# Optimization experiments

Hardware: AMD Instinct MI355X
Metric: run time of the kernel (lower is better)

## Reference

```python
import jax, jax.numpy as jnp
import numpy as np


def setup_inputs() -> dict:
    key = jax.random.key(0)
    k1, k2 = jax.random.split(key)
    B, D, H, W = 64, 64, 32, 32
    K = 1024
    z_e = jax.random.normal(k1, (B, D, H, W), dtype=jnp.float32)
    embedding = jax.random.normal(k2, (K, D), dtype=jnp.float32)
    return {"z_e": z_e, "embedding": embedding}


def reference(z_e, embedding):
    # Eval-mode forward of VectorQuantizer (EMA buffer updates are training-only state).
    B, D, H, W = z_e.shape
    K = embedding.shape[0]
    # (N, D) flattened encoder outputs, N = B*H*W
    flat = jnp.transpose(z_e, (0, 2, 3, 1)).reshape(-1, D)
    dist = (jnp.sum(flat * flat, axis=1, keepdims=True)
            + jnp.sum(embedding * embedding, axis=1)
            - 2.0 * flat @ embedding.T)  # (N, K)
    indices = jnp.argmin(dist, axis=1)  # (N,)
    z_q_flat = embedding[indices]  # (N, D) gather
    z_q = jnp.transpose(z_q_flat.reshape(B, H, W, D), (0, 3, 1, 2))
    # commitment loss: mse(z_e, sg(z_q))
    commitment_loss = jnp.mean((z_e - jax.lax.stop_gradient(z_q)) ** 2)
    # straight-through estimator
    z_q = z_e + jax.lax.stop_gradient(z_q - z_e)
    indices_bhw = indices.reshape(B, H, W)
    # fraction of codebook entries used this batch (jit-friendly unique count)
    used = jnp.zeros((K,), dtype=jnp.float32).at[indices].set(1.0)
    codebook_usage = jnp.sum(used) / K
    return z_q, commitment_loss, indices_bhw, codebook_usage
```

## Files before the change

### kernel.cpp

```cpp
#include <hip/hip_runtime.h>


#define DIMS 64
#define K_CODES 1024
#define N_QUERIES 65536
#define HW 1024
#define TOTAL_ELEMS 4194304
#define PLANE 4096

typedef __attribute__((ext_vector_type(8))) short v8s;
typedef __attribute__((ext_vector_type(4))) float f32x4;

__device__ inline unsigned short f2bf(float x) {
    union { float f; unsigned u; } v; v.f = x;
    unsigned r = v.u + 0x7fff + ((v.u >> 16) & 1);
    return (unsigned short)(r >> 16);
}
__device__ inline float bf2f(unsigned short h) {
    union { unsigned u; float f; } v; v.u = ((unsigned)h) << 16; return v.f;
}

__global__ void vq_prep(const float* __restrict__ emb, float* __restrict__ ws_norm,
                        int* __restrict__ ws_flags, float* __restrict__ ws_loss) {
    int k = blockIdx.x * 256 + threadIdx.x;
    const float4* row = (const float4*)(emb + k * DIMS);
    float s = 0.f;
#pragma unroll
    for (int i = 0; i < 16; ++i) {
        float4 v = row[i];
        s += v.x * v.x + v.y * v.y + v.z * v.z + v.w * v.w;
    }
    ws_norm[k] = s;
    ws_flags[k] = 0;
    if (k == 0) *ws_loss = 0.f;
}

#define MFMA16(A_, B_, C_) __builtin_amdgcn_mfma_f32_16x16x32_bf16(A_, B_, C_, 0, 0, 0)

__global__ __launch_bounds__(256, 2)
void vq_main(const float* __restrict__ z_e, const float* __restrict__ emb,
             const float* __restrict__ ws_norm, int* __restrict__ ws_flags,
             float* __restrict__ ws_loss, float* __restrict__ out) {
    __shared__ unsigned short ldsB[2][3 * PLANE];
    __shared__ int   fIdx[128];
    __shared__ float wsum[4];

    const int tid  = threadIdx.x;
    const int lane = tid & 63;
    const int wid  = tid >> 6;
    const int qbase = blockIdx.x * 128;
    const int b    = qbase >> 10;
    const int hwb  = qbase & (HW - 1);

    const int col  = lane & 15;
    const int qd   = lane >> 4;

    v8s afr[2][2][3];
    {
        const float* zb = z_e + b * (DIMS * HW);
#pragma unroll
        for (int rt = 0; rt < 2; ++rt) {
            int hwq = hwb + wid * 32 + rt * 16 + col;
#pragma unroll
            for (int kc = 0; kc < 2; ++kc) {
                int dbase = kc * 32 + qd * 8;
#pragma unroll
                for (int j = 0; j < 8; ++j) {
                    float x = zb[(dbase + j) * HW + hwq];
                    unsigned short h = f2bf(x);  float r1 = x - bf2f(h);
                    unsigned short m = f2bf(r1); float r2 = r1 - bf2f(m);
                    afr[rt][kc][0][j] = (short)h;
                    afr[rt][kc][1][j] = (short)m;
                    afr[rt][kc][2][j] = (short)f2bf(r2);
                }
            }
        }
    }

    float bestv[2][4];
    int   besti[2][4];
#pragma unroll
    for (int rt = 0; rt < 2; ++rt)
#pragma unroll
        for (int r = 0; r < 4; ++r) { bestv[rt][r] = 3.4e38f; besti[rt][r] = 0; }

    float4 regs[4];

    auto stage_loads = [&](int t) {
        const float4* src = (const float4*)(emb + t * 64 * DIMS);
#pragma unroll
        for (int i = 0; i < 4; ++i) regs[i] = src[tid + 256 * i];
    };
    auto stage_write = [&](int bb) {
        unsigned short* dst = &ldsB[bb][0];
#pragma unroll
        for (int i = 0; i < 4; ++i) {
            int e    = (tid + 256 * i) * 4;
            int code = e >> 6;
            int d    = e & 63;
            int o    = d >> 3;
            int sub  = d & 7;
            float xs[4] = {regs[i].x, regs[i].y, regs[i].z, regs[i].w};
            unsigned short h[4], mm_[4], l[4];
#pragma unroll
            for (int q = 0; q < 4; ++q) {
                float x = xs[q];
                unsigned short hh = f2bf(x);  float r1 = x - bf2f(hh);
                unsigned short mh = f2bf(r1); float r2 = r1 - bf2f(mh);
                h[q] = hh; mm_[q] = mh; l[q] = f2bf(r2);
            }
            int base = (o * 64 + code) * 8 + sub;
            uint2 uh, um, ul;
            uh.x = (unsigned)h[0]   | ((unsigned)h[1] << 16);
            uh.y = (unsigned)h[2]   | ((unsigned)h[3] << 16);
            um.x = (unsigned)mm_[0] | ((unsigned)mm_[1] << 16);
            um.y = (unsigned)mm_[2] | ((unsigned)mm_[3] << 16);
            ul.x = (unsigned)l[0]   | ((unsigned)l[1] << 16);
            ul.y = (unsigned)l[2]   | ((unsigned)l[3] << 16);
            *(uint2*)(dst + base)             = uh;
            *(uint2*)(dst + PLANE + base)     = um;
            *(uint2*)(dst + 2 * PLANE + base) = ul;
        }
    };

    stage_loads(0);
    stage_write(0);
    __syncthreads();

    for (int t = 0; t < 16; ++t) {
        const int cur = t & 1;
        if (t < 15) stage_loads(t + 1);
        const unsigned short* bufc = &ldsB[cur][0];
#pragma unroll
        for (int cs = 0; cs < 4; ++cs) {
            float nrm = ws_norm[t * 64 + cs * 16 + col];
            v8s bfr[2][3];
#pragma unroll
            for (int kc = 0; kc < 2; ++kc)
#pragma unroll
                for (int p = 0; p < 3; ++p)
                    bfr[kc][p] = *(const v8s*)(bufc + p * PLANE +
                                 (((kc * 4 + qd) * 64) + cs * 16 + col) * 8);
            f32x4 acc0 = {0.f, 0.f, 0.f, 0.f};
            f32x4 acc1 = {0.f, 0.f, 0.f, 0.f};
#pragma unroll
            for (int kc = 0; kc < 2; ++kc) {
                acc0 = MFMA16(afr[0][kc][0], bfr[kc][0], acc0);
                acc1 = MFMA16(afr[1][kc][0], bfr[kc][0], acc1);
                acc0 = MFMA16(afr[0][kc][0], bfr[kc][1], acc0);
                acc1 = MFMA16(afr[1][kc][0], bfr[kc][1], acc1);
                acc0 = MFMA16(afr[0][kc][1], bfr[kc][0], acc0);
                acc1 = MFMA16(afr[1][kc][1], bfr[kc][0], acc1);
                acc0 = MFMA16(afr[0][kc][1], bfr[kc][1], acc0);
                acc1 = MFMA16(afr[1][kc][1], bfr[kc][1], acc1);
                acc0 = MFMA16(afr[0][kc][0], bfr[kc][2], acc0);
                acc1 = MFMA16(afr[1][kc][0], bfr[kc][2], acc1);
                acc0 = MFMA16(afr[0][kc][2], bfr[kc][0], acc0);
                acc1 = MFMA16(afr[1][kc][2], bfr[kc][0], acc1);
            }
            int cbase = t * 64 + cs * 16 + col;
#pragma unroll
            for (int r = 0; r < 4; ++r) {
                float d0 = fmaf(-2.f, acc0[r], nrm);
                if (d0 < bestv[0][r]) { bestv[0][r] = d0; besti[0][r] = cbase; }
                float d1 = fmaf(-2.f, acc1[r], nrm);
                if (d1 < bestv[1][r]) { bestv[1][r] = d1; besti[1][r] = cbase; }
            }
        }
        if (t < 15) stage_write(1 - cur);
        __syncthreads();
    }

#pragma unroll
    for (int rt = 0; rt < 2; ++rt)
#pragma unroll
    for (int r = 0; r < 4; ++r) {
        float v = bestv[rt][r];
        int   idx = besti[rt][r];
#pragma unroll
        for (int m = 8; m >= 1; m >>= 1) {
            float ov = __shfl_xor(v, m, 64);
            int   oi = __shfl_xor(idx, m, 64);
            if (ov < v || (ov == v && oi < idx)) { v = ov; idx = oi; }
        }
        if (col == 0) {
            int q = wid * 32 + rt * 16 + qd * 4 + r;
            fIdx[q] = idx;
            out[TOTAL_ELEMS + 1 + qbase + q] = (float)idx;
            ws_flags[idx] = 1;
        }
    }
    __syncthreads();

    const int q  = tid & 127;
    const int dh = tid >> 7;
    const int n  = qbase + q;
    const int bb = n >> 10;
    const int hw = n & (HW - 1);
    const int myIdx = fIdx[q];
    const float* erow = emb + myIdx * DIMS;
    float lsum = 0.f;
#pragma unroll
    for (int it = 0; it < 32; ++it) {
        int d = it * 2 + dh;
        float v = erow[d];
        int   o = bb * (DIMS * HW) + d * HW + hw;
        float ze = z_e[o];
        out[o] = v;
        float df = ze - v;
        lsum = fmaf(df, df, lsum);
    }
#pragma unroll
    for (int off = 32; off > 0; off >>= 1) lsum += __shfl_down(lsum, off, 64);
    if (lane == 0) wsum[wid] = lsum;
    __syncthreads();
    if (tid == 0) atomicAdd(ws_loss, wsum[0] + wsum[1] + wsum[2] + wsum[3]);
}

__global__ void vq_final(const int* __restrict__ flags, const float* __restrict__ loss,
                         float* __restrict__ out) {
    __shared__ int cnt[256];
    int tid = threadIdx.x;
    int c = flags[tid] + flags[tid + 256] + flags[tid + 512] + flags[tid + 768];
    cnt[tid] = c;
    __syncthreads();
    for (int s = 128; s > 0; s >>= 1) {
        if (tid < s) cnt[tid] += cnt[tid + s];
        __syncthreads();
    }
    if (tid == 0) {
        out[TOTAL_ELEMS] = *loss / (float)TOTAL_ELEMS;
        out[TOTAL_ELEMS + 1 + N_QUERIES] = (float)cnt[0] / (float)K_CODES;
    }
}

extern "C" void kernel_launch(void* const* d_in, const int* in_sizes, int n_in,
                              void* d_out, int out_size, void* d_ws, size_t ws_size,
                              hipStream_t stream) {
    const float* z_e = (const float*)d_in[0];
    const float* emb = (const float*)d_in[1];
    float* out = (float*)d_out;
    float* ws_norm  = (float*)d_ws;
    int*   ws_flags = (int*)((char*)d_ws + 4096);
    float* ws_loss  = (float*)((char*)d_ws + 8192);

    vq_prep<<<4, 256, 0, stream>>>(emb, ws_norm, ws_flags, ws_loss);
    vq_main<<<512, 256, 0, stream>>>(z_e, emb, ws_norm, ws_flags, ws_loss, out);
    vq_final<<<1, 256, 0, stream>>>(ws_flags, ws_loss, out);
}
```

Baseline: 135.4 us.

## Fuse final reduction into main kernel, double block size, swizzle LDS codebook layout

Each block now has 512 threads and handles 256 queries, so a block stages each codebook tile once for twice as many queries. The B-operand LDS layout gets an XOR swizzle to reduce bank conflicts. The LDS write for the next tile is moved into the middle of the compute loop to overlap with MFMA work. Codebook usage becomes a per-block shared bitmask merged with atomicOr. A last-block-done counter computes the final loss and usage inside the main kernel, which removes the separate final launch. The cost is half as many blocks (256), which lowers parallelism across CUs, plus a thread fence and atomic counter per block.

```diff
diff --git a/kernel.cpp b/kernel.cpp
--- a/kernel.cpp
+++ b/kernel.cpp
@@ -7,6 +7,8 @@
 #define HW 1024
 #define TOTAL_ELEMS 4194304
 #define PLANE 4096
+#define NBLK 256
+#define QPB 256
 
 typedef __attribute__((ext_vector_type(8))) short v8s;
 typedef __attribute__((ext_vector_type(4))) float f32x4;
@@ -21,7 +23,8 @@
 }
 
 __global__ void vq_prep(const float* __restrict__ emb, float* __restrict__ ws_norm,
-                        int* __restrict__ ws_flags, float* __restrict__ ws_loss) {
+                        unsigned* __restrict__ ws_flags, float* __restrict__ ws_loss,
+                        int* __restrict__ ws_cnt) {
     int k = blockIdx.x * 256 + threadIdx.x;
     const float4* row = (const float4*)(emb + k * DIMS);
     float s = 0.f;
@@ -31,29 +34,34 @@
         s += v.x * v.x + v.y * v.y + v.z * v.z + v.w * v.w;
     }
     ws_norm[k] = s;
-    ws_flags[k] = 0;
-    if (k == 0) *ws_loss = 0.f;
+    if (k < 32) ws_flags[k] = 0u;
+    if (k == 0) { *ws_loss = 0.f; *ws_cnt = 0; }
 }
 
 #define MFMA16(A_, B_, C_) __builtin_amdgcn_mfma_f32_16x16x32_bf16(A_, B_, C_, 0, 0, 0)
 
-__global__ __launch_bounds__(256, 2)
+__global__ __launch_bounds__(512, 2)
 void vq_main(const float* __restrict__ z_e, const float* __restrict__ emb,
-             const float* __restrict__ ws_norm, int* __restrict__ ws_flags,
-             float* __restrict__ ws_loss, float* __restrict__ out) {
+             const float* __restrict__ ws_norm, unsigned* __restrict__ ws_flags,
+             float* __restrict__ ws_loss, int* __restrict__ ws_cnt,
+             float* __restrict__ out) {
     __shared__ unsigned short ldsB[2][3 * PLANE];
-    __shared__ int   fIdx[128];
-    __shared__ float wsum[4];
+    __shared__ int      fIdx[QPB];
+    __shared__ float    wsum[8];
+    __shared__ unsigned umask[32];
+    __shared__ int      lastBlk;
 
     const int tid  = threadIdx.x;
     const int lane = tid & 63;
     const int wid  = tid >> 6;
-    const int qbase = blockIdx.x * 128;
+    const int qbase = blockIdx.x * QPB;
     const int b    = qbase >> 10;
     const int hwb  = qbase & (HW - 1);
 
     const int col  = lane & 15;
     const int qd   = lane >> 4;
+
+    if (tid < 32) umask[tid] = 0u;
 
     v8s afr[2][2][3];
     {
@@ -84,18 +92,17 @@
 #pragma unroll
         for (int r = 0; r < 4; ++r) { bestv[rt][r] = 3.4e38f; besti[rt][r] = 0; }
 
-    float4 regs[4];
-
+    float4 regs[2];
     auto stage_loads = [&](int t) {
         const float4* src = (const float4*)(emb + t * 64 * DIMS);
 #pragma unroll
-        for (int i = 0; i < 4; ++i) regs[i] = src[tid + 256 * i];
+        for (int i = 0; i < 2; ++i) regs[i] = src[tid + 512 * i];
     };
-    auto stage_write = [&](int bb) {
-        unsigned short* dst = &ldsB[bb][0];
-#pragma unroll
-        for (int i = 0; i < 4; ++i) {
-            int e    = (tid + 256 * i) * 4;
+    auto stage_write = [&](int bb2) {
+        unsigned short* dst = &ldsB[bb2][0];
+#pragma unroll
+        for (int i = 0; i < 2; ++i) {
+            int e    = (tid + 512 * i) * 4;
             int code = e >> 6;
             int d    = e & 63;
             int o    = d >> 3;
@@ -109,7 +116,7 @@
                 unsigned short mh = f2bf(r1); float r2 = r1 - bf2f(mh);
                 h[q] = hh; mm_[q] = mh; l[q] = f2bf(r2);
             }
-            int base = (o * 64 + code) * 8 + sub;
+            int base = (o * 64 + (code ^ (o << 1))) * 8 + sub;
             uint2 uh, um, ul;
             uh.x = (unsigned)h[0]   | ((unsigned)h[1] << 16);
             uh.y = (unsigned)h[2]   | ((unsigned)h[3] << 16);
@@ -131,16 +138,18 @@
         const int cur = t & 1;
         if (t < 15) stage_loads(t + 1);
         const unsigned short* bufc = &ldsB[cur][0];
-#pragma unroll
-        for (int cs = 0; cs < 4; ++cs) {
+
+        auto csbody = [&](int cs) {
             float nrm = ws_norm[t * 64 + cs * 16 + col];
             v8s bfr[2][3];
 #pragma unroll
-            for (int kc = 0; kc < 2; ++kc)
+            for (int kc = 0; kc < 2; ++kc) {
+                int oct = kc * 4 + qd;
+                int slot = (cs * 16 + col) ^ (oct << 1);
 #pragma unroll
                 for (int p = 0; p < 3; ++p)
-                    bfr[kc][p] = *(const v8s*)(bufc + p * PLANE +
-                                 (((kc * 4 + qd) * 64) + cs * 16 + col) * 8);
+                    bfr[kc][p] = *(const v8s*)(bufc + p * PLANE + (oct * 64 + slot) * 8);
+            }
             f32x4 acc0 = {0.f, 0.f, 0.f, 0.f};
             f32x4 acc1 = {0.f, 0.f, 0.f, 0.f};
 #pragma unroll
@@ -166,8 +175,13 @@
                 float d1 = fmaf(-2.f, acc1[r], nrm);
                 if (d1 < bestv[1][r]) { bestv[1][r] = d1; besti[1][r] = cbase; }
             }
-        }
+        };
+
+        csbody(0);
+        csbody(1);
         if (t < 15) stage_write(1 - cur);
+        csbody(2);
+        csbody(3);
         __syncthreads();
     }
 
@@ -187,13 +201,13 @@
             int q = wid * 32 + rt * 16 + qd * 4 + r;
             fIdx[q] = idx;
             out[TOTAL_ELEMS + 1 + qbase + q] = (float)idx;
-            ws_flags[idx] = 1;
-        }
-    }
-    __syncthreads();
-
-    const int q  = tid & 127;
-    const int dh = tid >> 7;
+            atomicOr(&umask[idx >> 5], 1u << (idx & 31));
+        }
+    }
+    __syncthreads();
+
+    const int q  = tid & (QPB - 1);
+    const int dh = tid >> 8;
     const int n  = qbase + q;
     const int bb = n >> 10;
     const int hw = n & (HW - 1);
@@ -214,23 +228,29 @@
     for (int off = 32; off > 0; off >>= 1) lsum += __shfl_down(lsum, off, 64);
     if (lane == 0) wsum[wid] = lsum;
     __syncthreads();
-    if (tid == 0) atomicAdd(ws_loss, wsum[0] + wsum[1] + wsum[2] + wsum[3]);
-}
-
-__global__ void vq_final(const int* __restrict__ flags, const float* __restrict__ loss,
-                         float* __restrict__ out) {
-    __shared__ int cnt[256];
-    int tid = threadIdx.x;
-    int c = flags[tid] + flags[tid + 256] + flags[tid + 512] + flags[tid + 768];
-    cnt[tid] = c;
-    __syncthreads();
-    for (int s = 128; s > 0; s >>= 1) {
-        if (tid < s) cnt[tid] += cnt[tid + s];
-        __syncthreads();
-    }
+
+    if (tid < 32) atomicOr(&ws_flags[tid], umask[tid]);
     if (tid == 0) {
-        out[TOTAL_ELEMS] = *loss / (float)TOTAL_ELEMS;
-        out[TOTAL_ELEMS + 1 + N_QUERIES] = (float)cnt[0] / (float)K_CODES;
+        float bsum = 0.f;
+#pragma unroll
+        for (int w = 0; w < 8; ++w) bsum += wsum[w];
+        atomicAdd(ws_loss, bsum);
+    }
+    __threadfence();
+    if (tid == 0) lastBlk = (atomicAdd(ws_cnt, 1) == NBLK - 1) ? 1 : 0;
+    __syncthreads();
+    if (lastBlk) {
+        int c = 0;
+        if (tid < 32) c = __popc(atomicOr(&ws_flags[tid], 0u));
+        if (tid < 64) {
+#pragma unroll
+            for (int off = 32; off >= 1; off >>= 1) c += __shfl_down(c, off, 64);
+        }
+        if (tid == 0) {
+            float L = atomicAdd(ws_loss, 0.f);
+            out[TOTAL_ELEMS] = L / (float)TOTAL_ELEMS;
+            out[TOTAL_ELEMS + 1 + N_QUERIES] = (float)c / (float)K_CODES;
+        }
     }
 }
 
@@ -240,11 +260,12 @@
     const float* z_e = (const float*)d_in[0];
     const float* emb = (const float*)d_in[1];
     float* out = (float*)d_out;
-    float* ws_norm  = (float*)d_ws;
-    int*   ws_flags = (int*)((char*)d_ws + 4096);
-    float* ws_loss  = (float*)((char*)d_ws + 8192);
-
-    vq_prep<<<4, 256, 0, stream>>>(emb, ws_norm, ws_flags, ws_loss);
-    vq_main<<<512, 256, 0, stream>>>(z_e, emb, ws_norm, ws_flags, ws_loss, out);
-    vq_final<<<1, 256, 0, stream>>>(ws_flags, ws_loss, out);
-}
+    float*    ws_norm  = (float*)d_ws;
+    unsigned* ws_flags = (unsigned*)((char*)d_ws + 4096);
+    float*    ws_loss  = (float*)((char*)d_ws + 8192);
+    int*      ws_cnt   = (int*)((char*)d_ws + 8256);
+
+    vq_prep<<<4, 256, 0, stream>>>(emb, ws_norm, ws_flags, ws_loss, ws_cnt);
+    vq_main<<<NBLK, 512, 0, stream>>>(z_e, emb, ws_norm, ws_flags, ws_loss,
+                                      ws_cnt, out);
+}
```

After: 169.9 us. +25.5%, slower.
